# Kernel tuning notes

Measured on AMD Instinct MI355X. Metric: run time of the kernel, lower is better.

Reference implementation:

```python
import jax, jax.numpy as jnp
import numpy as np

D_MODEL = 4096
D_FF = 4 * D_MODEL
B, S = 2, 2048


def setup_inputs() -> dict:
    key = jax.random.key(0)
    kx, k1, kb1, k2, kb2 = jax.random.split(key, 5)
    s1 = 1.0 / np.sqrt(D_MODEL)
    s2 = 1.0 / np.sqrt(D_FF)
    return {
        "x": jax.random.normal(kx, (B, S, D_MODEL), dtype=jnp.float32),
        "W1": jax.random.normal(k1, (D_MODEL, D_FF), dtype=jnp.float32) * s1,
        "b1": jax.random.normal(kb1, (D_FF,), dtype=jnp.float32) * 0.01,
        "W2": jax.random.normal(k2, (D_FF, D_MODEL), dtype=jnp.float32) * s2,
        "b2": jax.random.normal(kb2, (D_MODEL,), dtype=jnp.float32) * 0.01,
    }


def reference(x, W1, b1, W2, b2):
    # FlashFFN: engine computes fc2(act(fc1(x) + b1)); host then nan-guards
    # and adds fc2_bias. GELU is the standard transformer FFN activation.
    orig_shape = x.shape
    flat_x = x.reshape(-1, D_MODEL)                      # [T, D]
    h = jax.nn.gelu(flat_x @ W1 + b1)                    # [T, 4D]
    y = h @ W2                                           # [T, D]
    y = jnp.nan_to_num(y, nan=0.0, posinf=0.0, neginf=0.0)
    return y.reshape(orig_shape) + b2
```

## Files before the change

### kernel.cpp

```cpp
#include <hip/hip_runtime.h>
#include <hip/hip_bf16.h>


using bf16 = __hip_bfloat16;
typedef __attribute__((ext_vector_type(4))) float floatx4;
typedef __attribute__((ext_vector_type(8))) short shortx8;

#define TOKENS 4096
#define DMODEL 4096
#define DFF    16384

__device__ __forceinline__ void gload_lds16(const void* g, void* l) {
  __builtin_amdgcn_global_load_lds(
      (const __attribute__((address_space(1))) unsigned int*)g,
      (__attribute__((address_space(3))) unsigned int*)l,
      16, 0, 0);
}

__device__ __forceinline__ unsigned lds_u32(const void* p) {
  return (unsigned)(unsigned long long)(const __attribute__((address_space(3))) char*)p;
}

__device__ __forceinline__ float gelu_tanh(float x) {
  float z = 0.7978845608028654f * (x + 0.044715f * x * x * x);
  float e = __expf(2.0f * z);
  float t = 1.0f - 2.0f / (e + 1.0f);
  return 0.5f * x * (1.0f + t);
}

#define DSR(dst, addr, off) \
  asm volatile("ds_read_b128 %0, %1 offset:" #off : "=v"(dst) : "v"(addr))

__global__ void cvt_f32_bf16(const float* __restrict__ in, bf16* __restrict__ out) {
  int i = (blockIdx.x * blockDim.x + threadIdx.x) * 8;
  float4 a = *(const float4*)(in + i);
  float4 b = *(const float4*)(in + i + 4);
  union { shortx8 v; bf16 h[8]; } r;
  r.h[0] = __float2bfloat16(a.x); r.h[1] = __float2bfloat16(a.y);
  r.h[2] = __float2bfloat16(a.z); r.h[3] = __float2bfloat16(a.w);
  r.h[4] = __float2bfloat16(b.x); r.h[5] = __float2bfloat16(b.y);
  r.h[6] = __float2bfloat16(b.z); r.h[7] = __float2bfloat16(b.w);
  *(shortx8*)(out + i) = r.v;
}

__global__ void transpose_cvt(const float* __restrict__ in, bf16* __restrict__ out,
                              int R, int C) {
  __shared__ float tile[64][65];
  const int c0 = blockIdx.x * 64, r0 = blockIdx.y * 64;
  const int t = threadIdx.x;
#pragma unroll
  for (int p = 0; p < 4; ++p) {
    int r = p * 16 + (t >> 4);
    int c = (t & 15) * 4;
    float4 v = *(const float4*)(in + (size_t)(r0 + r) * C + c0 + c);
    tile[r][c] = v.x; tile[r][c + 1] = v.y;
    tile[r][c + 2] = v.z; tile[r][c + 3] = v.w;
  }
  __syncthreads();
#pragma unroll
  for (int p = 0; p < 2; ++p) {
    int c = p * 32 + (t >> 3);
    int rb = (t & 7) * 8;
    union { shortx8 v; bf16 h[8]; } u;
#pragma unroll
    for (int j = 0; j < 8; ++j) u.h[j] = __float2bfloat16(tile[rb + j][c]);
    *(shortx8*)(out + (size_t)(c0 + c) * R + r0 + rb) = u.v;
  }
}

template <int FUSE_GELU>
__launch_bounds__(512, 2)
__global__ void gemm_bt(const bf16* __restrict__ A, const bf16* __restrict__ Bt,
                        const float* __restrict__ bias, void* __restrict__ Cout,
                        int M, int N, int K) {
  __shared__ __align__(16) bf16 As[2 * 2 * 128 * 64];
  __shared__ __align__(16) bf16 Bs[2 * 2 * 128 * 64];

  const int tid = threadIdx.x;
  const int wave = tid >> 6;
  const int lane = tid & 63;

  const int wg8  = blockIdx.x & 255;
  const int xcd  = wg8 & 7;
  const int slot = wg8 >> 3;
  const int m0 = (2 * xcd + (slot & 1)) * 256;
  const int n0 = ((blockIdx.x >> 8) * 16 + (slot >> 1)) * 256;

  const size_t Ks = (size_t)K;
  const int NT = K >> 6;

  const int swz = (lane & 7) ^ ((lane >> 3) & 7);
  const bf16* agp = A  + (size_t)(m0 + wave * 8 + (lane >> 3)) * Ks + swz * 8;
  const bf16* bgp = Bt + (size_t)(n0 + wave * 8 + (lane >> 3)) * Ks + swz * 8;

  const int wr = wave >> 2, wc = wave & 3;
  const int fr = lane & 15;
  const int q  = lane >> 4;
  const unsigned As0 = lds_u32(As);
  const unsigned Bs0 = lds_u32(Bs);
  const unsigned aK0 = As0 + (unsigned)((wr * 16 + fr) * 128 +
                       (((fr >> 2) & 1) * 64) + ((q ^ (fr & 3)) * 16));
  const unsigned aK1 = aK0 ^ 64u;
  const unsigned bK0 = Bs0 + (unsigned)((wc * 16 + fr) * 128 +
                       (((fr >> 2) & 1) * 64) + ((q ^ (fr & 3)) * 16));
  const unsigned bK1 = bK0 ^ 64u;

  floatx4 acc[8][4] = {};
  shortx8 A0[2][4], A1[2][4], B0[2][2], B1[2][2];

  {
    bf16* lA = As + wave * 512;
    bf16* lB = Bs + wave * 512;
    gload_lds16(agp,             lA);
    gload_lds16(agp +  64 * Ks,  lA + 4096);
    gload_lds16(bgp,             lB);
    gload_lds16(bgp +  64 * Ks,  lB + 4096);
    gload_lds16(agp + 128 * Ks,  lA + 8192);
    gload_lds16(agp + 192 * Ks,  lA + 12288);
    gload_lds16(bgp + 128 * Ks,  lB + 8192);
    gload_lds16(bgp + 192 * Ks,  lB + 12288);
    if (NT > 1) {
      bf16* lB1 = Bs + 16384 + wave * 512;
      const bf16* gB1 = bgp + 64;
      gload_lds16(gB1,           lB1);
      gload_lds16(gB1 + 64 * Ks, lB1 + 4096);
    }
  }
  if (NT > 1) asm volatile("s_waitcnt vmcnt(4)");
  else        asm volatile("s_waitcnt vmcnt(2)");
  __builtin_amdgcn_s_barrier();
  DSR(B0[0][0], bK0, 0); DSR(B0[0][1], bK0, 8192);
  DSR(B0[1][0], bK1, 0); DSR(B0[1][1], bK1, 8192);
  DSR(A0[0][0], aK0, 0);     DSR(A0[0][1], aK0, 4096);
  DSR(A0[0][2], aK0, 8192);  DSR(A0[0][3], aK0, 12288);
  DSR(A0[1][0], aK1, 0);     DSR(A0[1][1], aK1, 4096);
  DSR(A0[1][2], aK1, 8192);  DSR(A0[1][3], aK1, 12288);

  for (int t = 0; t < NT; ++t) {
    const unsigned dsel  = (unsigned)(t & 1) << 15;
    const unsigned dseln = (unsigned)((t + 1) & 1) << 15;
    const unsigned a0 = aK0 + dsel,  a1 = aK1 + dsel;
    const unsigned b0 = bK0 + dsel,  b1 = bK1 + dsel;
    const unsigned an0 = aK0 + dseln, an1 = aK1 + dseln;
    const unsigned bn0 = bK0 + dseln, bn1 = bK1 + dseln;
    const bool st  = (t + 1 < NT);
    const bool st2 = (t + 2 < NT);
    const bf16* gA = agp + (size_t)(t + 1) * 64;
    bf16* lA = As + ((t + 1) & 1) * 16384 + wave * 512;
    bf16* lB = Bs + ((t + 1) & 1) * 16384 + wave * 512;

    DSR(A1[0][0], a0, 16384); DSR(A1[0][1], a0, 20480);
    DSR(A1[0][2], a0, 24576); DSR(A1[0][3], a0, 28672);
    DSR(A1[1][0], a1, 16384); DSR(A1[1][1], a1, 20480);
    DSR(A1[1][2], a1, 24576); DSR(A1[1][3], a1, 28672);
    if (st) { gload_lds16(gA, lA); gload_lds16(gA + 64 * Ks, lA + 4096); }
    asm volatile("s_waitcnt lgkmcnt(8)");
    __builtin_amdgcn_sched_barrier(0);
    __builtin_amdgcn_s_setprio(1);
#pragma unroll
    for (int f = 0; f < 4; ++f)
#pragma unroll
      for (int n = 0; n < 2; ++n) {
        acc[f][n] = __builtin_amdgcn_mfma_f32_16x16x32_bf16(A0[0][f], B0[0][n], acc[f][n], 0, 0, 0);
        acc[f][n] = __builtin_amdgcn_mfma_f32_16x16x32_bf16(A0[1][f], B0[1][n], acc[f][n], 0, 0, 0);
      }
    __builtin_amdgcn_s_setprio(0);
    __builtin_amdgcn_sched_barrier(0);
    if (st) asm volatile("s_waitcnt vmcnt(4)");
    else    asm volatile("s_waitcnt vmcnt(0)");
    __builtin_amdgcn_s_barrier();

    DSR(B1[0][0], b0, 16384); DSR(B1[0][1], b0, 24576);
    DSR(B1[1][0], b1, 16384); DSR(B1[1][1], b1, 24576);
    if (st) { gload_lds16(gA + 128 * Ks, lA + 8192); gload_lds16(gA + 192 * Ks, lA + 12288); }
    asm volatile("s_waitcnt lgkmcnt(4)");
    __builtin_amdgcn_sched_barrier(0);
    __builtin_amdgcn_s_setprio(1);
#pragma unroll
    for (int f = 0; f < 4; ++f)
#pragma unroll
      for (int n = 0; n < 2; ++n) {
        acc[4 + f][n] = __builtin_amdgcn_mfma_f32_16x16x32_bf16(A1[0][f], B0[0][n], acc[4 + f][n], 0, 0, 0);
        acc[4 + f][n] = __builtin_amdgcn_mfma_f32_16x16x32_bf16(A1[1][f], B0[1][n], acc[4 + f][n], 0, 0, 0);
      }
    __builtin_amdgcn_s_setprio(0);
    __builtin_amdgcn_sched_barrier(0);
    if (st) asm volatile("s_waitcnt vmcnt(4)");
    __builtin_amdgcn_s_barrier();

    if (st) {
      const bf16* gB = bgp + (size_t)(t + 1) * 64;
      DSR(B0[0][0], bn0, 0); DSR(B0[0][1], bn0, 8192);
      DSR(B0[1][0], bn1, 0); DSR(B0[1][1], bn1, 8192);
      gload_lds16(gB + 128 * Ks, lB + 8192);
      gload_lds16(gB + 192 * Ks, lB + 12288);
      asm volatile("s_waitcnt lgkmcnt(4)");
    } else {
      asm volatile("s_waitcnt lgkmcnt(0)");
    }
    __builtin_amdgcn_sched_barrier(0);
    __builtin_amdgcn_s_setprio(1);
#pragma unroll
    for (int f = 0; f < 4; ++f)
#pragma unroll
      for (int n = 0; n < 2; ++n) {
        acc[4 + f][2 + n] = __builtin_amdgcn_mfma_f32_16x16x32_bf16(A1[0][f], B1[0][n], acc[4 + f][2 + n], 0, 0, 0);
        acc[4 + f][2 + n] = __builtin_amdgcn_mfma_f32_16x16x32_bf16(A1[1][f], B1[1][n], acc[4 + f][2 + n], 0, 0, 0);
      }
    __builtin_amdgcn_s_setprio(0);
    __builtin_amdgcn_sched_barrier(0);
    if (st) asm volatile("s_waitcnt vmcnt(4)");
    __builtin_amdgcn_s_barrier();

    if (st2) {
      const bf16* gB2 = bgp + (size_t)(t + 2) * 64;
      bf16* lB2 = Bs + (t & 1) * 16384 + wave * 512;
      gload_lds16(gB2,           lB2);
      gload_lds16(gB2 + 64 * Ks, lB2 + 4096);
    }
    __builtin_amdgcn_s_setprio(1);
#pragma unroll
    for (int f = 0; f < 4; ++f)
#pragma unroll
      for (int n = 0; n < 2; ++n) {
        acc[f][2 + n] = __builtin_amdgcn_mfma_f32_16x16x32_bf16(A0[0][f], B1[0][n], acc[f][2 + n], 0, 0, 0);
        acc[f][2 + n] = __builtin_amdgcn_mfma_f32_16x16x32_bf16(A0[1][f], B1[1][n], acc[f][2 + n], 0, 0, 0);
      }
    __builtin_amdgcn_s_setprio(0);
    __builtin_amdgcn_sched_barrier(0);
    if (st) {
      DSR(A0[0][0], an0, 0);     DSR(A0[0][1], an0, 4096);
      DSR(A0[0][2], an0, 8192);  DSR(A0[0][3], an0, 12288);
      DSR(A0[1][0], an1, 0);     DSR(A0[1][1], an1, 4096);
      DSR(A0[1][2], an1, 8192);  DSR(A0[1][3], an1, 12288);
    }
    if (st2)     asm volatile("s_waitcnt vmcnt(4)");
    else if (st) asm volatile("s_waitcnt vmcnt(2)");
    __builtin_amdgcn_s_barrier();
  }

  const int col0 = n0 + wc * 16 + fr;
  const int row0 = m0 + wr * 16 + (lane >> 4) * 4;
#pragma unroll
  for (int ni = 0; ni < 4; ++ni) {
    const int col = col0 + ni * 64;
    const float bv = bias[col];
#pragma unroll
    for (int mi = 0; mi < 8; ++mi) {
#pragma unroll
      for (int r = 0; r < 4; ++r) {
        const int row = row0 + mi * 32 + r;
        float v = acc[mi][ni][r];
        if (FUSE_GELU) {
          v = gelu_tanh(v + bv);
          ((bf16*)Cout)[(size_t)row * N + col] = __float2bfloat16(v);
        } else {
          if (!isfinite(v)) v = 0.0f;
          ((float*)Cout)[(size_t)row * N + col] = v + bv;
        }
      }
    }
  }
}

extern "C" void kernel_launch(void* const* d_in, const int* in_sizes, int n_in,
                              void* d_out, int out_size, void* d_ws, size_t ws_size,
                              hipStream_t stream) {
  const float* x  = (const float*)d_in[0];
  const float* W1 = (const float*)d_in[1];
  const float* b1 = (const float*)d_in[2];
  const float* W2 = (const float*)d_in[3];
  const float* b2 = (const float*)d_in[4];
  float* out = (float*)d_out;

  char* ws = (char*)d_ws;
  bf16* xb  = (bf16*)(ws);
  bf16* h   = (bf16*)(ws + (size_t)32  * 1024 * 1024);
  bf16* w1t = (bf16*)(ws + (size_t)160 * 1024 * 1024);
  bf16* w2t = (bf16*)(ws + (size_t)288 * 1024 * 1024);

  cvt_f32_bf16<<<(TOKENS * DMODEL / 8) / 256, 256, 0, stream>>>(x, xb);
  transpose_cvt<<<dim3(DFF / 64, DMODEL / 64), 256, 0, stream>>>(W1, w1t, DMODEL, DFF);
  transpose_cvt<<<dim3(DMODEL / 64, DFF / 64), 256, 0, stream>>>(W2, w2t, DFF, DMODEL);

  gemm_bt<1><<<dim3((DFF / 256) * (TOKENS / 256)), 512, 0, stream>>>(
      xb, w1t, b1, h, TOKENS, DFF, DMODEL);

  gemm_bt<0><<<dim3((DMODEL / 256) * (TOKENS / 256)), 512, 0, stream>>>(
      h, w2t, b2, out, TOKENS, DMODEL, DFF);
}
```

Baseline: 1.075 ms.

## Stagger LDS reads and MFMA clusters between two wave groups

Splits the eight waves into two groups. Group A issues its LDS reads and global-to-LDS loads before each MFMA cluster, while group B runs its MFMA cluster first and issues the reads after it. The aim is to spread LDS and issue traffic so one group's matrix work overlaps the other's memory phase, ping-pong style. It also reorders the MFMA chains so all K0 products come before the K1 products. Group B now waits for lgkmcnt(0) before computing, which may add stalls, and the stagger only pays off if the barriers allow the two groups to drift apart.

```diff
diff --git a/kernel.cpp b/kernel.cpp
--- a/kernel.cpp
+++ b/kernel.cpp
@@ -68,6 +68,53 @@
   }
 }
 
+#define READS_P1 \
+  DSR(A1[0][0], a0, 16384); DSR(A1[0][1], a0, 20480); \
+  DSR(A1[0][2], a0, 24576); DSR(A1[0][3], a0, 28672); \
+  DSR(A1[1][0], a1, 16384); DSR(A1[1][1], a1, 20480); \
+  DSR(A1[1][2], a1, 24576); DSR(A1[1][3], a1, 28672);
+#define STAGE_P1 \
+  if (st) { gload_lds16(gA, lA); gload_lds16(gA + 64 * Ks, lA + 4096); }
+#define READS_P2 \
+  DSR(B1[0][0], b0, 16384); DSR(B1[0][1], b0, 24576); \
+  DSR(B1[1][0], b1, 16384); DSR(B1[1][1], b1, 24576);
+#define STAGE_P2 \
+  if (st) { gload_lds16(gA + 128 * Ks, lA + 8192); \
+            gload_lds16(gA + 192 * Ks, lA + 12288); }
+#define READS_P3 \
+  DSR(B0[0][0], bn0, 0); DSR(B0[0][1], bn0, 8192); \
+  DSR(B0[1][0], bn1, 0); DSR(B0[1][1], bn1, 8192);
+#define STAGE_P3 \
+  { const bf16* gB = bgp + (size_t)(t + 1) * 64; \
+    gload_lds16(gB + 128 * Ks, lB + 8192); \
+    gload_lds16(gB + 192 * Ks, lB + 12288); }
+#define READS_P4 \
+  DSR(A0[0][0], an0, 0);     DSR(A0[0][1], an0, 4096); \
+  DSR(A0[0][2], an0, 8192);  DSR(A0[0][3], an0, 12288); \
+  DSR(A0[1][0], an1, 0);     DSR(A0[1][1], an1, 4096); \
+  DSR(A0[1][2], an1, 8192);  DSR(A0[1][3], an1, 12288);
+
+#define MFMA_CL(AF, BF, MO, NO) \
+  _Pragma("unroll") \
+  for (int f = 0; f < 4; ++f) \
+    _Pragma("unroll") \
+    for (int n = 0; n < 2; ++n) \
+      acc[(MO) + f][(NO) + n] = __builtin_amdgcn_mfma_f32_16x16x32_bf16( \
+          AF[0][f], BF[0][n], acc[(MO) + f][(NO) + n], 0, 0, 0); \
+  _Pragma("unroll") \
+  for (int f = 0; f < 4; ++f) \
+    _Pragma("unroll") \
+    for (int n = 0; n < 2; ++n) \
+      acc[(MO) + f][(NO) + n] = __builtin_amdgcn_mfma_f32_16x16x32_bf16( \
+          AF[1][f], BF[1][n], acc[(MO) + f][(NO) + n], 0, 0, 0);
+
+#define CLUSTER(AF, BF, MO, NO) \
+  __builtin_amdgcn_sched_barrier(0); \
+  __builtin_amdgcn_s_setprio(1); \
+  MFMA_CL(AF, BF, MO, NO) \
+  __builtin_amdgcn_s_setprio(0); \
+  __builtin_amdgcn_sched_barrier(0);
+
 template <int FUSE_GELU>
 __launch_bounds__(512, 2)
 __global__ void gemm_bt(const bf16* __restrict__ A, const bf16* __restrict__ Bt,
@@ -79,6 +126,7 @@
   const int tid = threadIdx.x;
   const int wave = tid >> 6;
   const int lane = tid & 63;
+  const bool grpA = (wave < 4);
 
   const int wg8  = blockIdx.x & 255;
   const int xcd  = wg8 & 7;
@@ -149,66 +197,44 @@
     bf16* lA = As + ((t + 1) & 1) * 16384 + wave * 512;
     bf16* lB = Bs + ((t + 1) & 1) * 16384 + wave * 512;
 
-    DSR(A1[0][0], a0, 16384); DSR(A1[0][1], a0, 20480);
-    DSR(A1[0][2], a0, 24576); DSR(A1[0][3], a0, 28672);
-    DSR(A1[1][0], a1, 16384); DSR(A1[1][1], a1, 20480);
-    DSR(A1[1][2], a1, 24576); DSR(A1[1][3], a1, 28672);
-    if (st) { gload_lds16(gA, lA); gload_lds16(gA + 64 * Ks, lA + 4096); }
-    asm volatile("s_waitcnt lgkmcnt(8)");
-    __builtin_amdgcn_sched_barrier(0);
-    __builtin_amdgcn_s_setprio(1);
-#pragma unroll
-    for (int f = 0; f < 4; ++f)
-#pragma unroll
-      for (int n = 0; n < 2; ++n) {
-        acc[f][n] = __builtin_amdgcn_mfma_f32_16x16x32_bf16(A0[0][f], B0[0][n], acc[f][n], 0, 0, 0);
-        acc[f][n] = __builtin_amdgcn_mfma_f32_16x16x32_bf16(A0[1][f], B0[1][n], acc[f][n], 0, 0, 0);
-      }
-    __builtin_amdgcn_s_setprio(0);
-    __builtin_amdgcn_sched_barrier(0);
+    if (grpA) {
+      READS_P1 STAGE_P1
+      asm volatile("s_waitcnt lgkmcnt(8)");
+      CLUSTER(A0, B0, 0, 0)
+    } else {
+      asm volatile("s_waitcnt lgkmcnt(0)");
+      CLUSTER(A0, B0, 0, 0)
+      READS_P1 STAGE_P1
+    }
     if (st) asm volatile("s_waitcnt vmcnt(4)");
     else    asm volatile("s_waitcnt vmcnt(0)");
     __builtin_amdgcn_s_barrier();
 
-    DSR(B1[0][0], b0, 16384); DSR(B1[0][1], b0, 24576);
-    DSR(B1[1][0], b1, 16384); DSR(B1[1][1], b1, 24576);
-    if (st) { gload_lds16(gA + 128 * Ks, lA + 8192); gload_lds16(gA + 192 * Ks, lA + 12288); }
-    asm volatile("s_waitcnt lgkmcnt(4)");
-    __builtin_amdgcn_sched_barrier(0);
-    __builtin_amdgcn_s_setprio(1);
-#pragma unroll
-    for (int f = 0; f < 4; ++f)
-#pragma unroll
-      for (int n = 0; n < 2; ++n) {
-        acc[4 + f][n] = __builtin_amdgcn_mfma_f32_16x16x32_bf16(A1[0][f], B0[0][n], acc[4 + f][n], 0, 0, 0);
-        acc[4 + f][n] = __builtin_amdgcn_mfma_f32_16x16x32_bf16(A1[1][f], B0[1][n], acc[4 + f][n], 0, 0, 0);
-      }
-    __builtin_amdgcn_s_setprio(0);
-    __builtin_amdgcn_sched_barrier(0);
+    if (grpA) {
+      READS_P2 STAGE_P2
+      asm volatile("s_waitcnt lgkmcnt(4)");
+      CLUSTER(A1, B0, 4, 0)
+    } else {
+      asm volatile("s_waitcnt lgkmcnt(0)");
+      CLUSTER(A1, B0, 4, 0)
+      READS_P2 STAGE_P2
+    }
     if (st) asm volatile("s_waitcnt vmcnt(4)");
     __builtin_amdgcn_s_barrier();
 
-    if (st) {
-      const bf16* gB = bgp + (size_t)(t + 1) * 64;
-      DSR(B0[0][0], bn0, 0); DSR(B0[0][1], bn0, 8192);
-      DSR(B0[1][0], bn1, 0); DSR(B0[1][1], bn1, 8192);
-      gload_lds16(gB + 128 * Ks, lB + 8192);
-      gload_lds16(gB + 192 * Ks, lB + 12288);
-      asm volatile("s_waitcnt lgkmcnt(4)");
+    if (grpA) {
+      if (st) {
+        READS_P3 STAGE_P3
+        asm volatile("s_waitcnt lgkmcnt(4)");
+      } else {
+        asm volatile("s_waitcnt lgkmcnt(0)");
+      }
+      CLUSTER(A1, B1, 4, 2)
     } else {
       asm volatile("s_waitcnt lgkmcnt(0)");
-    }
-    __builtin_amdgcn_sched_barrier(0);
-    __builtin_amdgcn_s_setprio(1);
-#pragma unroll
-    for (int f = 0; f < 4; ++f)
-#pragma unroll
-      for (int n = 0; n < 2; ++n) {
-        acc[4 + f][2 + n] = __builtin_amdgcn_mfma_f32_16x16x32_bf16(A1[0][f], B1[0][n], acc[4 + f][2 + n], 0, 0, 0);
-        acc[4 + f][2 + n] = __builtin_amdgcn_mfma_f32_16x16x32_bf16(A1[1][f], B1[1][n], acc[4 + f][2 + n], 0, 0, 0);
-      }
-    __builtin_amdgcn_s_setprio(0);
-    __builtin_amdgcn_sched_barrier(0);
+      CLUSTER(A1, B1, 4, 2)
+      if (st) { READS_P3 STAGE_P3 }
+    }
     if (st) asm volatile("s_waitcnt vmcnt(4)");
     __builtin_amdgcn_s_barrier();
 
@@ -218,22 +244,8 @@
       gload_lds16(gB2,           lB2);
       gload_lds16(gB2 + 64 * Ks, lB2 + 4096);
     }
-    __builtin_amdgcn_s_setprio(1);
-#pragma unroll
-    for (int f = 0; f < 4; ++f)
-#pragma unroll
-      for (int n = 0; n < 2; ++n) {
-        acc[f][2 + n] = __builtin_amdgcn_mfma_f32_16x16x32_bf16(A0[0][f], B1[0][n], acc[f][2 + n], 0, 0, 0);
-        acc[f][2 + n] = __builtin_amdgcn_mfma_f32_16x16x32_bf16(A0[1][f], B1[1][n], acc[f][2 + n], 0, 0, 0);
-      }
-    __builtin_amdgcn_s_setprio(0);
-    __builtin_amdgcn_sched_barrier(0);
-    if (st) {
-      DSR(A0[0][0], an0, 0);     DSR(A0[0][1], an0, 4096);
-      DSR(A0[0][2], an0, 8192);  DSR(A0[0][3], an0, 12288);
-      DSR(A0[1][0], an1, 0);     DSR(A0[1][1], an1, 4096);
-      DSR(A0[1][2], an1, 8192);  DSR(A0[1][3], an1, 12288);
-    }
+    CLUSTER(A0, B1, 0, 2)
+    if (st) { READS_P4 }
     if (st2)     asm volatile("s_waitcnt vmcnt(4)");
     else if (st) asm volatile("s_waitcnt vmcnt(2)");
     __builtin_amdgcn_s_barrier();
```

New measurement: 1.120 ms. 4.3% more time.

## Switch GEMM inner loop from 16x16x32 to 32x32x16 MFMA tiles

Applied to the files above, without the earlier changes.

Replaces the 16x16x32 bf16 MFMA fragments with 32x32x16 MFMA, changing the per-wave tile mapping, the LDS read addressing and swizzle, the accumulator layout, and the epilogue row/column mapping. Larger MFMA tiles need fewer LDS fragment reads per FLOP and fewer instructions issued, which is meant to raise matrix-core utilisation. The risk is LDS bank conflicts under the new swizzle and a wrong output mapping in the epilogue.

```diff
diff --git a/kernel.cpp b/kernel.cpp
--- a/kernel.cpp
+++ b/kernel.cpp
@@ -3,7 +3,7 @@
 
 
 using bf16 = __hip_bfloat16;
-typedef __attribute__((ext_vector_type(4))) float floatx4;
+typedef __attribute__((ext_vector_type(16))) float floatx16;
 typedef __attribute__((ext_vector_type(8))) short shortx8;
 
 #define TOKENS 4096
@@ -68,6 +68,18 @@
   }
 }
 
+#define CLUSTER32(AF, BF, MO, NO) \
+  __builtin_amdgcn_sched_barrier(0); \
+  __builtin_amdgcn_s_setprio(1); \
+  _Pragma("unroll") \
+  for (int ks = 0; ks < 4; ++ks) \
+    _Pragma("unroll") \
+    for (int mt = 0; mt < 2; ++mt) \
+      acc[(MO) + mt][NO] = __builtin_amdgcn_mfma_f32_32x32x16_bf16( \
+          AF[mt][ks], BF[ks], acc[(MO) + mt][NO], 0, 0, 0); \
+  __builtin_amdgcn_s_setprio(0); \
+  __builtin_amdgcn_sched_barrier(0);
+
 template <int FUSE_GELU>
 __launch_bounds__(512, 2)
 __global__ void gemm_bt(const bf16* __restrict__ A, const bf16* __restrict__ Bt,
@@ -94,19 +106,18 @@
   const bf16* bgp = Bt + (size_t)(n0 + wave * 8 + (lane >> 3)) * Ks + swz * 8;
 
   const int wr = wave >> 2, wc = wave & 3;
-  const int fr = lane & 15;
-  const int q  = lane >> 4;
+  const int l31 = lane & 31;
+  const int hi  = lane >> 5;
+  const int s   = lane & 7;
   const unsigned As0 = lds_u32(As);
   const unsigned Bs0 = lds_u32(Bs);
-  const unsigned aK0 = As0 + (unsigned)((wr * 16 + fr) * 128 +
-                       (((fr >> 2) & 1) * 64) + ((q ^ (fr & 3)) * 16));
-  const unsigned aK1 = aK0 ^ 64u;
-  const unsigned bK0 = Bs0 + (unsigned)((wc * 16 + fr) * 128 +
-                       (((fr >> 2) & 1) * 64) + ((q ^ (fr & 3)) * 16));
-  const unsigned bK1 = bK0 ^ 64u;
-
-  floatx4 acc[8][4] = {};
-  shortx8 A0[2][4], A1[2][4], B0[2][2], B1[2][2];
+  const unsigned aBase = As0 + (unsigned)((wr * 32 + l31) * 128 +
+                         ((hi ^ (s & 1)) << 4) + ((s >> 1) << 5));
+  const unsigned bBase = Bs0 + (unsigned)((wc * 32 + l31) * 128 +
+                         ((hi ^ (s & 1)) << 4) + ((s >> 1) << 5));
+
+  floatx16 acc[4][2] = {};
+  shortx8 A0[2][4], A1[2][4], B0[4], B1[4];
 
   {
     bf16* lA = As + wave * 512;
@@ -129,86 +140,72 @@
   if (NT > 1) asm volatile("s_waitcnt vmcnt(4)");
   else        asm volatile("s_waitcnt vmcnt(2)");
   __builtin_amdgcn_s_barrier();
-  DSR(B0[0][0], bK0, 0); DSR(B0[0][1], bK0, 8192);
-  DSR(B0[1][0], bK1, 0); DSR(B0[1][1], bK1, 8192);
-  DSR(A0[0][0], aK0, 0);     DSR(A0[0][1], aK0, 4096);
-  DSR(A0[0][2], aK0, 8192);  DSR(A0[0][3], aK0, 12288);
-  DSR(A0[1][0], aK1, 0);     DSR(A0[1][1], aK1, 4096);
-  DSR(A0[1][2], aK1, 8192);  DSR(A0[1][3], aK1, 12288);
+  {
+    unsigned bx;
+    bx = bBase;        DSR(B0[0], bx, 0);
+    bx = bBase ^ 32u;  DSR(B0[1], bx, 0);
+    bx = bBase ^ 64u;  DSR(B0[2], bx, 0);
+    bx = bBase ^ 96u;  DSR(B0[3], bx, 0);
+    unsigned ax;
+    ax = aBase;        DSR(A0[0][0], ax, 0); DSR(A0[1][0], ax, 8192);
+    ax = aBase ^ 32u;  DSR(A0[0][1], ax, 0); DSR(A0[1][1], ax, 8192);
+    ax = aBase ^ 64u;  DSR(A0[0][2], ax, 0); DSR(A0[1][2], ax, 8192);
+    ax = aBase ^ 96u;  DSR(A0[0][3], ax, 0); DSR(A0[1][3], ax, 8192);
+  }
 
   for (int t = 0; t < NT; ++t) {
     const unsigned dsel  = (unsigned)(t & 1) << 15;
     const unsigned dseln = (unsigned)((t + 1) & 1) << 15;
-    const unsigned a0 = aK0 + dsel,  a1 = aK1 + dsel;
-    const unsigned b0 = bK0 + dsel,  b1 = bK1 + dsel;
-    const unsigned an0 = aK0 + dseln, an1 = aK1 + dseln;
-    const unsigned bn0 = bK0 + dseln, bn1 = bK1 + dseln;
+    const unsigned a0d = aBase + dsel;
+    const unsigned b0d = bBase + dsel;
     const bool st  = (t + 1 < NT);
     const bool st2 = (t + 2 < NT);
     const bf16* gA = agp + (size_t)(t + 1) * 64;
     bf16* lA = As + ((t + 1) & 1) * 16384 + wave * 512;
     bf16* lB = Bs + ((t + 1) & 1) * 16384 + wave * 512;
 
-    DSR(A1[0][0], a0, 16384); DSR(A1[0][1], a0, 20480);
-    DSR(A1[0][2], a0, 24576); DSR(A1[0][3], a0, 28672);
-    DSR(A1[1][0], a1, 16384); DSR(A1[1][1], a1, 20480);
-    DSR(A1[1][2], a1, 24576); DSR(A1[1][3], a1, 28672);
+    {
+      unsigned ax;
+      ax = a0d;        DSR(A1[0][0], ax, 16384); DSR(A1[1][0], ax, 24576);
+      ax = a0d ^ 32u;  DSR(A1[0][1], ax, 16384); DSR(A1[1][1], ax, 24576);
+      ax = a0d ^ 64u;  DSR(A1[0][2], ax, 16384); DSR(A1[1][2], ax, 24576);
+      ax = a0d ^ 96u;  DSR(A1[0][3], ax, 16384); DSR(A1[1][3], ax, 24576);
+    }
     if (st) { gload_lds16(gA, lA); gload_lds16(gA + 64 * Ks, lA + 4096); }
     asm volatile("s_waitcnt lgkmcnt(8)");
-    __builtin_amdgcn_sched_barrier(0);
-    __builtin_amdgcn_s_setprio(1);
-#pragma unroll
-    for (int f = 0; f < 4; ++f)
-#pragma unroll
-      for (int n = 0; n < 2; ++n) {
-        acc[f][n] = __builtin_amdgcn_mfma_f32_16x16x32_bf16(A0[0][f], B0[0][n], acc[f][n], 0, 0, 0);
-        acc[f][n] = __builtin_amdgcn_mfma_f32_16x16x32_bf16(A0[1][f], B0[1][n], acc[f][n], 0, 0, 0);
-      }
-    __builtin_amdgcn_s_setprio(0);
-    __builtin_amdgcn_sched_barrier(0);
+    CLUSTER32(A0, B0, 0, 0)
     if (st) asm volatile("s_waitcnt vmcnt(4)");
     else    asm volatile("s_waitcnt vmcnt(0)");
     __builtin_amdgcn_s_barrier();
 
-    DSR(B1[0][0], b0, 16384); DSR(B1[0][1], b0, 24576);
-    DSR(B1[1][0], b1, 16384); DSR(B1[1][1], b1, 24576);
+    {
+      unsigned bx;
+      bx = b0d;        DSR(B1[0], bx, 16384);
+      bx = b0d ^ 32u;  DSR(B1[1], bx, 16384);
+      bx = b0d ^ 64u;  DSR(B1[2], bx, 16384);
+      bx = b0d ^ 96u;  DSR(B1[3], bx, 16384);
+    }
     if (st) { gload_lds16(gA + 128 * Ks, lA + 8192); gload_lds16(gA + 192 * Ks, lA + 12288); }
     asm volatile("s_waitcnt lgkmcnt(4)");
-    __builtin_amdgcn_sched_barrier(0);
-    __builtin_amdgcn_s_setprio(1);
-#pragma unroll
-    for (int f = 0; f < 4; ++f)
-#pragma unroll
-      for (int n = 0; n < 2; ++n) {
-        acc[4 + f][n] = __builtin_amdgcn_mfma_f32_16x16x32_bf16(A1[0][f], B0[0][n], acc[4 + f][n], 0, 0, 0);
-        acc[4 + f][n] = __builtin_amdgcn_mfma_f32_16x16x32_bf16(A1[1][f], B0[1][n], acc[4 + f][n], 0, 0, 0);
-      }
-    __builtin_amdgcn_s_setprio(0);
-    __builtin_amdgcn_sched_barrier(0);
+    CLUSTER32(A1, B0, 2, 0)
     if (st) asm volatile("s_waitcnt vmcnt(4)");
     __builtin_amdgcn_s_barrier();
 
     if (st) {
       const bf16* gB = bgp + (size_t)(t + 1) * 64;
-      DSR(B0[0][0], bn0, 0); DSR(B0[0][1], bn0, 8192);
-      DSR(B0[1][0], bn1, 0); DSR(B0[1][1], bn1, 8192);
+      const unsigned bnd = bBase + dseln;
+      unsigned bx;
+      bx = bnd;        DSR(B0[0], bx, 0);
+      bx = bnd ^ 32u;  DSR(B0[1], bx, 0);
+      bx = bnd ^ 64u;  DSR(B0[2], bx, 0);
+      bx = bnd ^ 96u;  DSR(B0[3], bx, 0);
       gload_lds16(gB + 128 * Ks, lB + 8192);
       gload_lds16(gB + 192 * Ks, lB + 12288);
       asm volatile("s_waitcnt lgkmcnt(4)");
     } else {
       asm volatile("s_waitcnt lgkmcnt(0)");
     }
-    __builtin_amdgcn_sched_barrier(0);
-    __builtin_amdgcn_s_setprio(1);
-#pragma unroll
-    for (int f = 0; f < 4; ++f)
-#pragma unroll
-      for (int n = 0; n < 2; ++n) {
-        acc[4 + f][2 + n] = __builtin_amdgcn_mfma_f32_16x16x32_bf16(A1[0][f], B1[0][n], acc[4 + f][2 + n], 0, 0, 0);
-        acc[4 + f][2 + n] = __builtin_amdgcn_mfma_f32_16x16x32_bf16(A1[1][f], B1[1][n], acc[4 + f][2 + n], 0, 0, 0);
-      }
-    __builtin_amdgcn_s_setprio(0);
-    __builtin_amdgcn_sched_barrier(0);
+    CLUSTER32(A1, B1, 2, 1)
     if (st) asm volatile("s_waitcnt vmcnt(4)");
     __builtin_amdgcn_s_barrier();
 
@@ -218,39 +215,33 @@
       gload_lds16(gB2,           lB2);
       gload_lds16(gB2 + 64 * Ks, lB2 + 4096);
     }
-    __builtin_amdgcn_s_setprio(1);
-#pragma unroll
-    for (int f = 0; f < 4; ++f)
-#pragma unroll
-      for (int n = 0; n < 2; ++n) {
-        acc[f][2 + n] = __builtin_amdgcn_mfma_f32_16x16x32_bf16(A0[0][f], B1[0][n], acc[f][2 + n], 0, 0, 0);
-        acc[f][2 + n] = __builtin_amdgcn_mfma_f32_16x16x32_bf16(A0[1][f], B1[1][n], acc[f][2 + n], 0, 0, 0);
-      }
-    __builtin_amdgcn_s_setprio(0);
-    __builtin_amdgcn_sched_barrier(0);
+    CLUSTER32(A0, B1, 0, 1)
     if (st) {
-      DSR(A0[0][0], an0, 0);     DSR(A0[0][1], an0, 4096);
-      DSR(A0[0][2], an0, 8192);  DSR(A0[0][3], an0, 12288);
-      DSR(A0[1][0], an1, 0);     DSR(A0[1][1], an1, 4096);
-      DSR(A0[1][2], an1, 8192);  DSR(A0[1][3], an1, 12288);
+      const unsigned and_ = aBase + dseln;
+      unsigned ax;
+      ax = and_;        DSR(A0[0][0], ax, 0); DSR(A0[1][0], ax, 8192);
+      ax = and_ ^ 32u;  DSR(A0[0][1], ax, 0); DSR(A0[1][1], ax, 8192);
+      ax = and_ ^ 64u;  DSR(A0[0][2], ax, 0); DSR(A0[1][2], ax, 8192);
+      ax = and_ ^ 96u;  DSR(A0[0][3], ax, 0); DSR(A0[1][3], ax, 8192);
     }
     if (st2)     asm volatile("s_waitcnt vmcnt(4)");
     else if (st) asm volatile("s_waitcnt vmcnt(2)");
     __builtin_amdgcn_s_barrier();
   }
 
-  const int col0 = n0 + wc * 16 + fr;
-  const int row0 = m0 + wr * 16 + (lane >> 4) * 4;
-#pragma unroll
-  for (int ni = 0; ni < 4; ++ni) {
-    const int col = col0 + ni * 64;
+  const int colb = n0 + wc * 32 + l31;
+  const int rowb = m0 + wr * 32 + 4 * hi;
+#pragma unroll
+  for (int nt = 0; nt < 2; ++nt) {
+    const int col = colb + nt * 128;
     const float bv = bias[col];
 #pragma unroll
-    for (int mi = 0; mi < 8; ++mi) {
-#pragma unroll
-      for (int r = 0; r < 4; ++r) {
-        const int row = row0 + mi * 32 + r;
-        float v = acc[mi][ni][r];
+    for (int mt = 0; mt < 4; ++mt) {
+      const int rb2 = rowb + (mt & 1) * 64 + (mt >> 1) * 128;
+#pragma unroll
+      for (int reg = 0; reg < 16; ++reg) {
+        const int row = rb2 + (reg & 3) + 8 * (reg >> 2);
+        float v = acc[mt][nt][reg];
         if (FUSE_GELU) {
           v = gelu_tanh(v + bv);
           ((bf16*)Cout)[(size_t)row * N + col] = __float2bfloat16(v);
```

After: 1.250 ms. 16.3% more time.
